# Optimization experiments

Measured on AMD Instinct MI355X. Metric: run time of the kernel, lower is better.

## Reference

```python
import jax, jax.numpy as jnp
import numpy as np

N = 50000
E = 800000
IN_F = 128
HID = 64
CLS = 40


def _seg_softmax(logits, seg, n):
    m = jax.ops.segment_max(logits, seg, num_segments=n)
    e = jnp.exp(logits - m[seg])
    s = jax.ops.segment_sum(e, seg, num_segments=n)
    return e / s[seg]


def _layer(x, src, dst, norm, W, aw, ab, sw, sb, alpha, bias, n):
    h = x @ W.T                                  # [N, HID]
    hs = h[src]                                  # [Etot, HID] gather
    ht = h[dst]
    s = hs * norm[:, None]
    t = ht * norm[:, None]
    s_aggr = jax.ops.segment_sum(hs, src, num_segments=n)
    t_aggr = jax.ops.segment_sum(ht, dst, num_segments=n)
    sim = jax.nn.leaky_relu(
        jnp.concatenate([s, t], axis=-1) @ aw.T + ab, 0.2)[:, 0]
    a = _seg_softmax(sim, src, n)
    nsim = jax.nn.leaky_relu(
        jnp.concatenate([s_aggr[src], t_aggr[dst]], axis=-1) @ sw.T + sb, 0.2)[:, 0]
    struct = _seg_softmax(nsim, src, n)
    w = alpha[0] * a + (1.0 - alpha[0]) * struct  # [Etot]
    msg = w[:, None] * hs                         # message(x_j, norm)
    out = jax.ops.segment_max(msg, dst, num_segments=n)  # aggr='max' at target
    return out + bias


def setup_inputs() -> dict:
    key = jax.random.key(0)
    ks = jax.random.split(key, 16)
    x = jax.random.normal(ks[0], (N, IN_F), dtype=jnp.float32)
    edge_index = jax.random.randint(ks[1], (2, E), 0, N, dtype=jnp.int32)
    norm = jax.random.uniform(ks[2], (E + N,), dtype=jnp.float32)
    def lin(k, o, i):
        return jax.random.normal(k, (o, i), dtype=jnp.float32) / np.sqrt(i)
    return {
        "x": x, "edge_index": edge_index, "norm": norm,
        "lin_w0": lin(ks[3], HID, IN_F), "lin_w1": lin(ks[4], HID, HID),
        "a_w0": lin(ks[5], 1, 2 * HID), "a_b0": jnp.zeros((1,), jnp.float32),
        "a_w1": lin(ks[6], 1, 2 * HID), "a_b1": jnp.zeros((1,), jnp.float32),
        "s_w0": lin(ks[7], 1, 2 * HID), "s_b0": jnp.zeros((1,), jnp.float32),
        "s_w1": lin(ks[8], 1, 2 * HID), "s_b1": jnp.zeros((1,), jnp.float32),
        "alpha0": jnp.array([0.5], jnp.float32), "alpha1": jnp.array([0.5], jnp.float32),
        "bias0": jnp.zeros((HID,), jnp.float32), "bias1": jnp.zeros((HID,), jnp.float32),
        "out_w": lin(ks[9], CLS, HID), "out_b": jnp.zeros((CLS,), jnp.float32),
    }


def reference(x, edge_index, norm, lin_w0, lin_w1, a_w0, a_b0, a_w1, a_b1,
              s_w0, s_b0, s_w1, s_b1, alpha0, alpha1, bias0, bias1, out_w, out_b):
    n = x.shape[0]
    loop = jnp.arange(n, dtype=edge_index.dtype)
    src = jnp.concatenate([edge_index[0], loop])  # add_self_loops
    dst = jnp.concatenate([edge_index[1], loop])
    h = _layer(x, src, dst, norm, lin_w0, a_w0, a_b0, s_w0, s_b0, alpha0, bias0, n)
    h = jax.nn.relu(h)
    h = _layer(h, src, dst, norm, lin_w1, a_w1, a_b1, s_w1, s_b1, alpha1, bias1, n)
    h = jax.nn.relu(h)
    logits = h @ out_w.T + out_b
    return jax.nn.log_softmax(logits, axis=-1)
```

## Files before the change

kernel.cpp:

```cpp
#include <hip/hip_runtime.h>
#include <hip/hip_fp16.h>
#include <cstddef>

#define HID 64
#define CLS 40

__device__ __forceinline__ float lrelu(float x) { return x >= 0.f ? x : 0.2f * x; }

__device__ __forceinline__ float wmax32(float v) {
#pragma unroll
    for (int o = 16; o > 0; o >>= 1) v = fmaxf(v, __shfl_xor(v, o));
    return v;
}
__device__ __forceinline__ float wsum32(float v) {
#pragma unroll
    for (int o = 16; o > 0; o >>= 1) v += __shfl_xor(v, o);
    return v;
}

template <int K, bool APPLY>
__device__ __forceinline__ void gemm_body(const float* __restrict__ X,
                                          const float* __restrict__ W,
                                          const float* __restrict__ aw,
                                          const float* __restrict__ sw,
                                          const int* __restrict__ degS,
                                          const int* __restrict__ degD,
                                          __half* __restrict__ Hh, size_t hN, int R,
                                          float* __restrict__ ds,
                                          float* __restrict__ dssw,
                                          float2* __restrict__ dtp,
                                          float* __restrict__ dtraw,
                                          float* __restrict__ d2raw,
                                          float* __restrict__ d3raw,
                                          int n, int brow, int tid) {
    constexpr int STR = K + 4;
    __shared__ float Wl[HID * STR];
    __shared__ float awl[128];
    __shared__ float swl[128];
    for (int i = tid; i < HID * K; i += 256) {
        int c = i / K, k = i % K;
        Wl[c * STR + k] = W[i];
    }
    if (tid < 128) awl[tid] = aw[tid];
    else swl[tid - 128] = sw[tid - 128];
    __syncthreads();
    int r = brow * 64 + (tid >> 2);
    int seg = tid & 3;
    if (r >= n) return;
    float acc[16];
#pragma unroll
    for (int c = 0; c < 16; c++) acc[c] = 0.f;
    const float* xr = X + (size_t)r * K;
    const float* wb = &Wl[4 * seg * STR];
    for (int k = 0; k < K; k += 4) {
        float4 xv = *reinterpret_cast<const float4*>(xr + k);
#pragma unroll
        for (int c = 0; c < 16; c++) {
            int crel = 16 * (c >> 2) + (c & 3);
            float4 wv = *reinterpret_cast<const float4*>(wb + crel * STR + k);
            acc[c] += xv.x * wv.x + xv.y * wv.y + xv.z * wv.z + xv.w * wv.w;
        }
    }
    float d0 = 0.f, d1 = 0.f, d2 = 0.f, d3 = 0.f;
#pragma unroll
    for (int c = 0; c < 16; c++) {
        int cc = 16 * (c >> 2) + 4 * seg + (c & 3);
        d0 += acc[c] * awl[cc];
        d1 += acc[c] * awl[64 + cc];
        d2 += acc[c] * swl[cc];
        d3 += acc[c] * swl[64 + cc];
    }
    uint2 stv[4];
#pragma unroll
    for (int t = 0; t < 4; t++) {
        union { __half2 h2[2]; uint2 u; } st;
        st.h2[0] = __floats2half2_rn(acc[4 * t], acc[4 * t + 1]);
        st.h2[1] = __floats2half2_rn(acc[4 * t + 2], acc[4 * t + 3]);
        stv[t] = st.u;
    }
    for (int rep = 0; rep < R; rep++) {
        __half* hb = Hh + (size_t)rep * hN + (size_t)r * HID + 4 * seg;
#pragma unroll
        for (int t = 0; t < 4; t++)
            *reinterpret_cast<uint2*>(hb + 16 * t) = stv[t];
    }
    d0 += __shfl_xor(d0, 1); d0 += __shfl_xor(d0, 2);
    d1 += __shfl_xor(d1, 1); d1 += __shfl_xor(d1, 2);
    d2 += __shfl_xor(d2, 1); d2 += __shfl_xor(d2, 2);
    d3 += __shfl_xor(d3, 1); d3 += __shfl_xor(d3, 2);
    if (seg == 0) {
        ds[r] = d0;
        if (APPLY) {
            dssw[r] = (float)(degS[r] + 1) * d2;
            float2 v = make_float2(d1, (float)(degD[r] + 1) * d3);
            for (int rep = 0; rep < 8; rep++) dtp[(size_t)rep * n + r] = v;
        } else {
            dtraw[r] = d1;
            d2raw[r] = d2;
            d3raw[r] = d3;
        }
    }
}

__global__ __launch_bounds__(256) void k_fused0(const float* __restrict__ x,
                                                const float* __restrict__ w0,
                                                const float* __restrict__ aw,
                                                const float* __restrict__ sw,
                                                __half* __restrict__ Hh, size_t hN, int R,
                                                float* __restrict__ ds,
                                                float* __restrict__ dtraw,
                                                float* __restrict__ d2raw,
                                                float* __restrict__ d3raw,
                                                const int* __restrict__ ei,
                                                int* degS, int* degD,
                                                unsigned* __restrict__ ranks,
                                                int n, int E, int gb) {
    if ((int)blockIdx.x < gb) {
        gemm_body<128, false>(x, w0, aw, sw, nullptr, nullptr, Hh, hN, R, ds,
                              nullptr, nullptr, dtraw, d2raw, d3raw,
                              n, blockIdx.x, threadIdx.x);
    } else {
        int t = (blockIdx.x - gb) * 256 + threadIdx.x;
        int stride = (gridDim.x - gb) * 256;
        for (int e = t; e < E; e += stride) {
            int s = ei[e], d = ei[E + e];
            unsigned rs = (unsigned)atomicAdd(&degS[s], 1);
            unsigned rd = (unsigned)atomicAdd(&degD[d], 1);
            ranks[e] = rs | (rd << 16);
        }
    }
}

__global__ __launch_bounds__(256) void k_gemm1(const float* __restrict__ X,
                                               const float* __restrict__ W,
                                               const float* __restrict__ aw,
                                               const float* __restrict__ sw,
                                               const int* __restrict__ degS,
                                               const int* __restrict__ degD,
                                               __half* __restrict__ Hh, size_t hN, int R,
                                               float* __restrict__ ds,
                                               float* __restrict__ dssw,
                                               float2* __restrict__ dtp,
                                               int n) {
    gemm_body<64, true>(X, W, aw, sw, degS, degD, Hh, hN, R, ds, dssw, dtp,
                        nullptr, nullptr, nullptr, n, blockIdx.x, threadIdx.x);
}

__global__ __launch_bounds__(1024) void k_scanA(const int* __restrict__ degS,
                                                const int* __restrict__ degD,
                                                const float* __restrict__ d2raw,
                                                const float* __restrict__ d3raw,
                                                const float* __restrict__ dtraw,
                                                int* __restrict__ offS,
                                                int* __restrict__ offD,
                                                int* __restrict__ bsum,
                                                float* __restrict__ dssw,
                                                float2* __restrict__ dtp,
                                                int n, int nb) {
    __shared__ int buf[2][1024];
    int which = (int)blockIdx.x >= nb;
    const int* deg = which ? degD : degS;
    int* off = which ? offD : offS;
    int b = blockIdx.x - (which ? nb : 0);
    int tid = threadIdx.x;
    int i = b * 1024 + tid;
    int v = (i < n) ? deg[i] + 1 : 0;
    int cur = 0;
    buf[0][tid] = v;
    __syncthreads();
#pragma unroll
    for (int o = 1; o < 1024; o <<= 1) {
        int t = buf[cur][tid];
        if (tid >= o) t += buf[cur][tid - o];
        buf[cur ^ 1][tid] = t;
        cur ^= 1;
        __syncthreads();
    }
    if (i < n) off[i] = buf[cur][tid];
    if (tid == 1023) bsum[which * 64 + b] = buf[cur][1023];
    if (!which && i < n) {
        dssw[i] = (float)(degS[i] + 1) * d2raw[i];
        float2 vv = make_float2(dtraw[i], (float)(degD[i] + 1) * d3raw[i]);
        for (int rep = 0; rep < 8; rep++) dtp[(size_t)rep * n + i] = vv;
    }
}

__global__ __launch_bounds__(1024) void k_scanC(const int* __restrict__ degS,
                                                const int* __restrict__ degD,
                                                int* __restrict__ offS,
                                                int* __restrict__ offD,
                                                const int* __restrict__ bsum,
                                                int n, int total, int nb) {
    __shared__ int basesum;
    int which = (int)blockIdx.x >= nb;
    const int* deg = which ? degD : degS;
    int* off = which ? offD : offS;
    int b = blockIdx.x - (which ? nb : 0);
    if (threadIdx.x < 64) {
        int v = ((int)threadIdx.x < b) ? bsum[which * 64 + threadIdx.x] : 0;
#pragma unroll
        for (int o = 32; o > 0; o >>= 1) v += __shfl_xor(v, o);
        if (threadIdx.x == 0) basesum = v;
    }
    __syncthreads();
    int i = b * 1024 + threadIdx.x;
    if (i < n) off[i] = off[i] - (deg[i] + 1) + basesum;
    if (i == 0) off[n] = total;
}

__global__ __launch_bounds__(256) void k_slots(const int* __restrict__ ei,
                                               const unsigned* __restrict__ ranks,
                                               const int* __restrict__ offS,
                                               const int* __restrict__ offD,
                                               int2* __restrict__ slots,
                                               int Et, int E) {
    int e = blockIdx.x * 256 + threadIdx.x;
    if (e >= Et) return;
    if (e < E) {
        int s = ei[e], d = ei[E + e];
        unsigned ur = ranks[e];
        slots[e] = make_int2(offS[s] + (int)(ur & 0xffffu),
                             offD[d] + (int)(ur >> 16));
    } else {
        int v = e - E;
        slots[e] = make_int2(offS[v + 1] - 1, offD[v + 1] - 1);
    }
}

__global__ __launch_bounds__(256) void k_scatter(const int* __restrict__ ei,
                                                 const float* __restrict__ norm,
                                                 const int2* __restrict__ slots,
                                                 const int* __restrict__ offS,
                                                 const int* __restrict__ offD,
                                                 int2* __restrict__ csrS,
                                                 int2* __restrict__ csrD,
                                                 int Et, int E, int N) {
    int grp = blockIdx.x & 7;
    int lo = (int)(((long long)grp * N) / 8);
    int hi = (int)(((long long)(grp + 1) * N) / 8);
    int sLo = offS[lo], sHi = offS[hi];
    int dLo = offD[lo], dHi = offD[hi];
    int start = (blockIdx.x >> 3) * 256 + threadIdx.x;
    int stride = (gridDim.x >> 3) * 256;
    for (int e = start; e < Et; e += stride) {
        int2 sl = slots[e];
        bool doS = (sl.x >= sLo) & (sl.x < sHi);
        bool doD = (sl.y >= dLo) & (sl.y < dHi);
        if (doS | doD) {
            int nb = __float_as_int(norm[e]);
            if (doS) {
                int d = (e < E) ? ei[E + e] : e - E;
                csrS[sl.x] = make_int2(d, nb);
            }
            if (doD) {
                int s = (e < E) ? ei[e] : e - E;
                csrD[sl.y] = make_int2(s, sl.x);
            }
        }
    }
}

__global__ __launch_bounds__(256) void k_soft(const int* __restrict__ offS,
                                              const int2* __restrict__ csrS,
                                              const float* __restrict__ ds,
                                              const float* __restrict__ dssw,
                                              const float2* __restrict__ dtp,
                                              const float* __restrict__ ab,
                                              const float* __restrict__ sb,
                                              const float* __restrict__ alpha,
                                              float* __restrict__ w, int n) {
    const float2* dtpc = dtp + (size_t)(blockIdx.x & 7) * n;
    int node = blockIdx.x * 8 + (threadIdx.x >> 5);
    int lane = threadIdx.x & 31;
    if (node >= n) return;
    int beg = offS[node];
    int deg = offS[node + 1] - beg;
    float ds_s = ds[node], dssw_s = dssw[node];
    float ab0 = ab[0], sb0 = sb[0], al = alpha[0];

    if (deg <= 32) {
        bool valid = lane < deg;
        float sim = -INFINITY, nsim = -INFINITY;
        int pos = beg + lane;
        if (valid) {
            int2 c = csrS[pos];
            float nr = __int_as_float(c.y);
            float2 p = dtpc[c.x];
            sim = lrelu(nr * (ds_s + p.x) + ab0);
            nsim = lrelu(dssw_s + p.y + sb0);
        }
        float mAv = wmax32(sim), mNv = wmax32(nsim);
        float eA = valid ? expf(sim - mAv) : 0.f;
        float eN = valid ? expf(nsim - mNv) : 0.f;
        float sAv = wsum32(eA), sNv = wsum32(eN);
        if (valid) w[pos] = al * eA / sAv + (1.f - al) * eN / sNv;
    } else {
        float mAv = -INFINITY, mNv = -INFINITY;
        for (int base = 0; base < deg; base += 32) {
            int idx = base + lane;
            if (idx < deg) {
                int2 c = csrS[beg + idx];
                float nr = __int_as_float(c.y);
                float2 p = dtpc[c.x];
                mAv = fmaxf(mAv, lrelu(nr * (ds_s + p.x) + ab0));
                mNv = fmaxf(mNv, lrelu(dssw_s + p.y + sb0));
            }
        }
        mAv = wmax32(mAv);
        mNv = wmax32(mNv);
        float a = 0.f, bb = 0.f;
        for (int base = 0; base < deg; base += 32) {
            int idx = base + lane;
            if (idx < deg) {
                int2 c = csrS[beg + idx];
                float nr = __int_as_float(c.y);
                float2 p = dtpc[c.x];
                a += expf(lrelu(nr * (ds_s + p.x) + ab0) - mAv);
                bb += expf(lrelu(dssw_s + p.y + sb0) - mNv);
            }
        }
        float sAv = wsum32(a);
        float sNv = wsum32(bb);
        for (int base = 0; base < deg; base += 32) {
            int idx = base + lane;
            if (idx < deg) {
                int2 c = csrS[beg + idx];
                float nr = __int_as_float(c.y);
                float2 p = dtpc[c.x];
                float eA = expf(lrelu(nr * (ds_s + p.x) + ab0) - mAv);
                float eN = expf(lrelu(dssw_s + p.y + sb0) - mNv);
                w[beg + idx] = al * eA / sAv + (1.f - al) * eN / sNv;
            }
        }
    }
}

__global__ __launch_bounds__(256) void k_aggr(const int* __restrict__ offD,
                                              const int2* __restrict__ csrD,
                                              const float* __restrict__ w,
                                              const __half* __restrict__ HhR,
                                              size_t hN, int R,
                                              const float* __restrict__ bias,
                                              float* __restrict__ out, int n) {
    const __half* Hh = HhR + (size_t)(blockIdx.x & (R - 1)) * hN;
    int wid = threadIdx.x >> 6;
    int lane = threadIdx.x & 63;
    int half = lane >> 5;
    int l32 = lane & 31;
    int node = (blockIdx.x * 4 + wid) * 2 + half;
    bool nvalid = node < n;
    int beg = 0, deg = 0;
    if (nvalid) { beg = offD[node]; deg = offD[node + 1] - beg; }
    int degOther = __shfl(deg, lane ^ 32);
    int maxdeg = max(deg, degOther);
    float ml0 = -INFINITY, ml1 = -INFINITY, ml2 = -INFINITY, ml3 = -INFINITY;
    float mh0 = -INFINITY, mh1 = -INFINITY, mh2 = -INFINITY, mh3 = -INFINITY;
    for (int base = 0; base < maxdeg; base += 32) {
        int idx = base + l32;
        int s = 0;
        float wv = 0.f;
        if (idx < deg) {
            int2 c = csrD[beg + idx];
            s = c.x;
            wv = w[c.y];
        }
        int cnt = min(32, maxdeg - base);
        int cnt4 = cnt & ~3;
        int bl = half << 5;
        for (int j = 0; j < cnt4; j += 4) {
            int s0 = __shfl(s, bl + j),     s1 = __shfl(s, bl + j + 1),
                s2 = __shfl(s, bl + j + 2), s3 = __shfl(s, bl + j + 3);
            float w0 = __shfl(wv, bl + j),     w1 = __shfl(wv, bl + j + 1),
                  w2 = __shfl(wv, bl + j + 2), w3 = __shfl(wv, bl + j + 3);
            float hl0 = __half2float(Hh[(size_t)s0 * HID + l32]);
            float hh0 = __half2float(Hh[(size_t)s0 * HID + 32 + l32]);
            float hl1 = __half2float(Hh[(size_t)s1 * HID + l32]);
            float hh1 = __half2float(Hh[(size_t)s1 * HID + 32 + l32]);
            float hl2 = __half2float(Hh[(size_t)s2 * HID + l32]);
            float hh2 = __half2float(Hh[(size_t)s2 * HID + 32 + l32]);
            float hl3 = __half2float(Hh[(size_t)s3 * HID + l32]);
            float hh3 = __half2float(Hh[(size_t)s3 * HID + 32 + l32]);
            if (base + j < deg)     { ml0 = fmaxf(ml0, w0 * hl0); mh0 = fmaxf(mh0, w0 * hh0); }
            if (base + j + 1 < deg) { ml1 = fmaxf(ml1, w1 * hl1); mh1 = fmaxf(mh1, w1 * hh1); }
            if (base + j + 2 < deg) { ml2 = fmaxf(ml2, w2 * hl2); mh2 = fmaxf(mh2, w2 * hh2); }
            if (base + j + 3 < deg) { ml3 = fmaxf(ml3, w3 * hl3); mh3 = fmaxf(mh3, w3 * hh3); }
        }
        for (int j = cnt4; j < cnt; j++) {
            int sj = __shfl(s, bl + j);
            float wj = __shfl(wv, bl + j);
            float hl = __half2float(Hh[(size_t)sj * HID + l32]);
            float hh = __half2float(Hh[(size_t)sj * HID + 32 + l32]);
            if (base + j < deg) { ml0 = fmaxf(ml0, wj * hl); mh0 = fmaxf(mh0, wj * hh); }
        }
    }
    if (nvalid) {
        float mlo = fmaxf(fmaxf(ml0, ml1), fmaxf(ml2, ml3));
        float mhi = fmaxf(fmaxf(mh0, mh1), fmaxf(mh2, mh3));
        out[(size_t)node * HID + l32] = fmaxf(mlo + bias[l32], 0.f);
        out[(size_t)node * HID + 32 + l32] = fmaxf(mhi + bias[32 + l32], 0.f);
    }
}

__global__ __launch_bounds__(256) void k_logits(const float* __restrict__ H,
                                                const float* __restrict__ OW,
                                                const float* __restrict__ OB,
                                                float* __restrict__ out, int n) {
    __shared__ float Wl[CLS * HID];
    __shared__ float Bl[CLS];
    int tid = threadIdx.x;
    for (int i = tid; i < CLS * HID; i += 256) Wl[i] = OW[i];
    if (tid < CLS) Bl[tid] = OB[tid];
    __syncthreads();
    int node = blockIdx.x * 32 + (tid >> 3);
    int g = tid & 7;
    if (node >= n) return;
    const float* h = H + (size_t)node * HID;
    float hreg[HID];
#pragma unroll
    for (int k = 0; k < HID; k += 4) {
        float4 hv = *reinterpret_cast<const float4*>(h + k);
        hreg[k] = hv.x; hreg[k + 1] = hv.y; hreg[k + 2] = hv.z; hreg[k + 3] = hv.w;
    }
    float lg[5];
#pragma unroll
    for (int j = 0; j < 5; j++) {
        int c = g * 5 + j;
        float a = 0.f;
        const float* wr = &Wl[c * HID];
#pragma unroll
        for (int k = 0; k < HID; k++) a += hreg[k] * wr[k];
        lg[j] = a + Bl[c];
    }
    float m = lg[0];
#pragma unroll
    for (int j = 1; j < 5; j++) m = fmaxf(m, lg[j]);
    m = fmaxf(m, __shfl_xor(m, 1));
    m = fmaxf(m, __shfl_xor(m, 2));
    m = fmaxf(m, __shfl_xor(m, 4));
    float s = 0.f;
#pragma unroll
    for (int j = 0; j < 5; j++) s += expf(lg[j] - m);
    s += __shfl_xor(s, 1);
    s += __shfl_xor(s, 2);
    s += __shfl_xor(s, 4);
    float lse = m + logf(s);
    float* o = out + (size_t)node * CLS + g * 5;
#pragma unroll
    for (int j = 0; j < 5; j++) o[j] = lg[j] - lse;
}

extern "C" void kernel_launch(void* const* d_in, const int* in_sizes, int n_in,
                              void* d_out, int out_size, void* d_ws, size_t ws_size,
                              hipStream_t stream) {
    const float* x   = (const float*)d_in[0];
    const int*   ei  = (const int*)d_in[1];
    const float* nrm = (const float*)d_in[2];
    const float* w0  = (const float*)d_in[3];
    const float* w1  = (const float*)d_in[4];
    const float* aw0 = (const float*)d_in[5];
    const float* ab0 = (const float*)d_in[6];
    const float* aw1 = (const float*)d_in[7];
    const float* ab1 = (const float*)d_in[8];
    const float* sw0 = (const float*)d_in[9];
    const float* sb0 = (const float*)d_in[10];
    const float* sw1 = (const float*)d_in[11];
    const float* sb1 = (const float*)d_in[12];
    const float* al0 = (const float*)d_in[13];
    const float* al1 = (const float*)d_in[14];
    const float* b0  = (const float*)d_in[15];
    const float* b1  = (const float*)d_in[16];
    const float* ow  = (const float*)d_in[17];
    const float* ob  = (const float*)d_in[18];
    float* out = (float*)d_out;

    int N = in_sizes[0] / 128;
    int E = in_sizes[1] / 2;
    int Et = E + N;

    char* base = (char*)d_ws;
    size_t off = 0;
    auto alloc = [&](size_t bytes) {
        void* p = base + off;
        off += (bytes + 255) & ~(size_t)255;
        return p;
    };
    int* degS = (int*)alloc(N * 4);
    int* degD = (int*)alloc(N * 4);
    int* offS = (int*)alloc((N + 1) * 4);
    int* offD = (int*)alloc((N + 1) * 4);
    int* bsum = (int*)alloc(128 * 4);
    unsigned* ranks = (unsigned*)alloc((size_t)E * 4);
    int2* slots = (int2*)alloc((size_t)Et * 8);
    int2* csrS = (int2*)alloc((size_t)Et * 8);
    int2* csrD = (int2*)alloc((size_t)Et * 8);
    float* wgt   = (float*)alloc((size_t)Et * 4);
    float* ds    = (float*)alloc(N * 4);
    float* dssw  = (float*)alloc(N * 4);
    float* dtraw = (float*)alloc(N * 4);
    float* d2raw = (float*)alloc(N * 4);
    float* d3raw = (float*)alloc(N * 4);
    float2* dtp  = (float2*)alloc((size_t)N * 8 * 8);
    float* lay   = (float*)alloc((size_t)N * HID * 4);

    size_t hbytes = (size_t)N * HID * 2;
    size_t rem = (off < ws_size) ? ws_size - off : hbytes;
    int R = 1;
    while (R < 8 && (size_t)(R * 2) * hbytes <= rem) R <<= 1;
    __half* HhR = (__half*)alloc(hbytes * R);
    size_t hN = (size_t)N * HID;

    int nbScan = (N + 1023) / 1024;
    int nbW2 = (N + 7) / 8;
    int nbS = (N + 7) / 8;
    int gb = (N + 63) / 64;
    int cnb = (E + 1023) / 1024;

    hipMemsetAsync(degS, 0, (size_t)N * 4, stream);
    hipMemsetAsync(degD, 0, (size_t)N * 4, stream);
    k_fused0<<<gb + cnb, 256, 0, stream>>>(x, w0, aw0, sw0, HhR, hN, R, ds,
                                           dtraw, d2raw, d3raw,
                                           ei, degS, degD, ranks, N, E, gb);
    k_scanA<<<2 * nbScan, 1024, 0, stream>>>(degS, degD, d2raw, d3raw, dtraw,
                                             offS, offD, bsum, dssw, dtp,
                                             N, nbScan);
    k_scanC<<<2 * nbScan, 1024, 0, stream>>>(degS, degD, offS, offD, bsum,
                                             N, Et, nbScan);
    k_slots<<<(Et + 255) / 256, 256, 0, stream>>>(ei, ranks, offS, offD,
                                                  slots, Et, E);
    k_scatter<<<2048, 256, 0, stream>>>(ei, nrm, slots, offS, offD,
                                        csrS, csrD, Et, E, N);

    k_soft<<<nbS, 256, 0, stream>>>(offS, csrS, ds, dssw, dtp,
                                    ab0, sb0, al0, wgt, N);
    k_aggr<<<nbW2, 256, 0, stream>>>(offD, csrD, wgt, HhR, hN, R, b0, lay, N);

    k_gemm1<<<gb, 256, 0, stream>>>(lay, w1, aw1, sw1, degS, degD,
                                    HhR, hN, R, ds, dssw, dtp, N);
    k_soft<<<nbS, 256, 0, stream>>>(offS, csrS, ds, dssw, dtp,
                                    ab1, sb1, al1, wgt, N);
    k_aggr<<<nbW2, 256, 0, stream>>>(offD, csrD, wgt, HhR, hN, R, b1, lay, N);

    k_logits<<<(N + 31) / 32, 256, 0, stream>>>(lay, ow, ob, out, N);
}
```

Measured before the change: 294.0 us.

## Fuse logits into final aggregation, store edge weights and layer output in fp16

Edge weights are now stored as fp16 and replicated R times alongside the replicated H copies, so each aggr block reads from its own replica. The layer-1 output is stored as fp16 and read by gemm1 through a half-precision load path. The separate logits/log-softmax kernel is folded into the second aggregation kernel, which computes the output projection from shared memory. This cuts memory traffic and one launch, at the cost of precision loss in weights and activations, more replicated-write work in k_soft, and an extra block-wide sync in the final aggregation.

```diff
diff --git a/kernel.cpp b/kernel.cpp
--- a/kernel.cpp
+++ b/kernel.cpp
@@ -18,8 +18,8 @@
     return v;
 }
 
-template <int K, bool APPLY>
-__device__ __forceinline__ void gemm_body(const float* __restrict__ X,
+template <int K, bool APPLY, typename XT>
+__device__ __forceinline__ void gemm_body(const XT* __restrict__ X,
                                           const float* __restrict__ W,
                                           const float* __restrict__ aw,
                                           const float* __restrict__ sw,
@@ -50,10 +50,18 @@
     float acc[16];
 #pragma unroll
     for (int c = 0; c < 16; c++) acc[c] = 0.f;
-    const float* xr = X + (size_t)r * K;
+    const XT* xr = X + (size_t)r * K;
     const float* wb = &Wl[4 * seg * STR];
     for (int k = 0; k < K; k += 4) {
-        float4 xv = *reinterpret_cast<const float4*>(xr + k);
+        float4 xv;
+        if constexpr (sizeof(XT) == 4) {
+            xv = *reinterpret_cast<const float4*>(xr + k);
+        } else {
+            __half2 a = *reinterpret_cast<const __half2*>(xr + k);
+            __half2 b = *reinterpret_cast<const __half2*>(xr + k + 2);
+            xv = make_float4(__low2float(a), __high2float(a),
+                             __low2float(b), __high2float(b));
+        }
 #pragma unroll
         for (int c = 0; c < 16; c++) {
             int crel = 16 * (c >> 2) + (c & 3);
@@ -116,9 +124,9 @@
                                                 unsigned* __restrict__ ranks,
                                                 int n, int E, int gb) {
     if ((int)blockIdx.x < gb) {
-        gemm_body<128, false>(x, w0, aw, sw, nullptr, nullptr, Hh, hN, R, ds,
-                              nullptr, nullptr, dtraw, d2raw, d3raw,
-                              n, blockIdx.x, threadIdx.x);
+        gemm_body<128, false, float>(x, w0, aw, sw, nullptr, nullptr, Hh, hN, R, ds,
+                                     nullptr, nullptr, dtraw, d2raw, d3raw,
+                                     n, blockIdx.x, threadIdx.x);
     } else {
         int t = (blockIdx.x - gb) * 256 + threadIdx.x;
         int stride = (gridDim.x - gb) * 256;
@@ -131,7 +139,7 @@
     }
 }
 
-__global__ __launch_bounds__(256) void k_gemm1(const float* __restrict__ X,
+__global__ __launch_bounds__(256) void k_gemm1(const __half* __restrict__ X,
                                                const float* __restrict__ W,
                                                const float* __restrict__ aw,
                                                const float* __restrict__ sw,
@@ -142,8 +150,8 @@
                                                float* __restrict__ dssw,
                                                float2* __restrict__ dtp,
                                                int n) {
-    gemm_body<64, true>(X, W, aw, sw, degS, degD, Hh, hN, R, ds, dssw, dtp,
-                        nullptr, nullptr, nullptr, n, blockIdx.x, threadIdx.x);
+    gemm_body<64, true, __half>(X, W, aw, sw, degS, degD, Hh, hN, R, ds, dssw, dtp,
+                                nullptr, nullptr, nullptr, n, blockIdx.x, threadIdx.x);
 }
 
 __global__ __launch_bounds__(1024) void k_scanA(const int* __restrict__ degS,
@@ -268,7 +276,8 @@
                                               const float* __restrict__ ab,
                                               const float* __restrict__ sb,
                                               const float* __restrict__ alpha,
-                                              float* __restrict__ w, int n) {
+                                              __half* __restrict__ wgtR, int wN, int R,
+                                              int n) {
     const float2* dtpc = dtp + (size_t)(blockIdx.x & 7) * n;
     int node = blockIdx.x * 8 + (threadIdx.x >> 5);
     int lane = threadIdx.x & 31;
@@ -293,7 +302,10 @@
         float eA = valid ? expf(sim - mAv) : 0.f;
         float eN = valid ? expf(nsim - mNv) : 0.f;
         float sAv = wsum32(eA), sNv = wsum32(eN);
-        if (valid) w[pos] = al * eA / sAv + (1.f - al) * eN / sNv;
+        if (valid) {
+            __half hv = __float2half(al * eA / sAv + (1.f - al) * eN / sNv);
+            for (int rep = 0; rep < R; rep++) wgtR[(size_t)rep * wN + pos] = hv;
+        }
     } else {
         float mAv = -INFINITY, mNv = -INFINITY;
         for (int base = 0; base < deg; base += 32) {
@@ -329,24 +341,42 @@
                 float2 p = dtpc[c.x];
                 float eA = expf(lrelu(nr * (ds_s + p.x) + ab0) - mAv);
                 float eN = expf(lrelu(dssw_s + p.y + sb0) - mNv);
-                w[beg + idx] = al * eA / sAv + (1.f - al) * eN / sNv;
+                __half hv = __float2half(al * eA / sAv + (1.f - al) * eN / sNv);
+                for (int rep = 0; rep < R; rep++)
+                    wgtR[(size_t)rep * wN + beg + idx] = hv;
             }
         }
     }
 }
 
+template <bool FINAL>
 __global__ __launch_bounds__(256) void k_aggr(const int* __restrict__ offD,
                                               const int2* __restrict__ csrD,
-                                              const float* __restrict__ w,
-                                              const __half* __restrict__ HhR,
-                                              size_t hN, int R,
+                                              const __half* __restrict__ wgtR, int wN,
+                                              const __half* __restrict__ HhR, size_t hN,
+                                              int R,
                                               const float* __restrict__ bias,
-                                              float* __restrict__ out, int n) {
-    const __half* Hh = HhR + (size_t)(blockIdx.x & (R - 1)) * hN;
+                                              const float* __restrict__ OW,
+                                              const float* __restrict__ OB,
+                                              __half* __restrict__ outH,
+                                              float* __restrict__ outF, int n) {
+    __shared__ float WlT[FINAL ? HID * CLS : 1];
+    __shared__ float Bl[FINAL ? CLS : 1];
+    __shared__ float hbuf[FINAL ? 8 : 1][FINAL ? HID : 1];
+    if (FINAL) {
+        for (int i = threadIdx.x; i < CLS * HID; i += 256)
+            WlT[(i & (HID - 1)) * CLS + (i >> 6)] = OW[i];
+        if (threadIdx.x < CLS) Bl[threadIdx.x] = OB[threadIdx.x];
+        __syncthreads();
+    }
+    int cpy = blockIdx.x & (R - 1);
+    const __half* Hh = HhR + (size_t)cpy * hN;
+    const __half* wg = wgtR + (size_t)cpy * wN;
     int wid = threadIdx.x >> 6;
     int lane = threadIdx.x & 63;
     int half = lane >> 5;
     int l32 = lane & 31;
+    int halfId = threadIdx.x >> 5;
     int node = (blockIdx.x * 4 + wid) * 2 + half;
     bool nvalid = node < n;
     int beg = 0, deg = 0;
@@ -362,7 +392,7 @@
         if (idx < deg) {
             int2 c = csrD[beg + idx];
             s = c.x;
-            wv = w[c.y];
+            wv = __half2float(wg[c.y]);
         }
         int cnt = min(32, maxdeg - base);
         int cnt4 = cnt & ~3;
@@ -393,60 +423,34 @@
             if (base + j < deg) { ml0 = fmaxf(ml0, wj * hl); mh0 = fmaxf(mh0, wj * hh); }
         }
     }
-    if (nvalid) {
-        float mlo = fmaxf(fmaxf(ml0, ml1), fmaxf(ml2, ml3));
-        float mhi = fmaxf(fmaxf(mh0, mh1), fmaxf(mh2, mh3));
-        out[(size_t)node * HID + l32] = fmaxf(mlo + bias[l32], 0.f);
-        out[(size_t)node * HID + 32 + l32] = fmaxf(mhi + bias[32 + l32], 0.f);
-    }
-}
-
-__global__ __launch_bounds__(256) void k_logits(const float* __restrict__ H,
-                                                const float* __restrict__ OW,
-                                                const float* __restrict__ OB,
-                                                float* __restrict__ out, int n) {
-    __shared__ float Wl[CLS * HID];
-    __shared__ float Bl[CLS];
-    int tid = threadIdx.x;
-    for (int i = tid; i < CLS * HID; i += 256) Wl[i] = OW[i];
-    if (tid < CLS) Bl[tid] = OB[tid];
-    __syncthreads();
-    int node = blockIdx.x * 32 + (tid >> 3);
-    int g = tid & 7;
-    if (node >= n) return;
-    const float* h = H + (size_t)node * HID;
-    float hreg[HID];
-#pragma unroll
-    for (int k = 0; k < HID; k += 4) {
-        float4 hv = *reinterpret_cast<const float4*>(h + k);
-        hreg[k] = hv.x; hreg[k + 1] = hv.y; hreg[k + 2] = hv.z; hreg[k + 3] = hv.w;
-    }
-    float lg[5];
-#pragma unroll
-    for (int j = 0; j < 5; j++) {
-        int c = g * 5 + j;
-        float a = 0.f;
-        const float* wr = &Wl[c * HID];
-#pragma unroll
-        for (int k = 0; k < HID; k++) a += hreg[k] * wr[k];
-        lg[j] = a + Bl[c];
-    }
-    float m = lg[0];
-#pragma unroll
-    for (int j = 1; j < 5; j++) m = fmaxf(m, lg[j]);
-    m = fmaxf(m, __shfl_xor(m, 1));
-    m = fmaxf(m, __shfl_xor(m, 2));
-    m = fmaxf(m, __shfl_xor(m, 4));
-    float s = 0.f;
-#pragma unroll
-    for (int j = 0; j < 5; j++) s += expf(lg[j] - m);
-    s += __shfl_xor(s, 1);
-    s += __shfl_xor(s, 2);
-    s += __shfl_xor(s, 4);
-    float lse = m + logf(s);
-    float* o = out + (size_t)node * CLS + g * 5;
-#pragma unroll
-    for (int j = 0; j < 5; j++) o[j] = lg[j] - lse;
+    float mlo = fmaxf(fmaxf(ml0, ml1), fmaxf(ml2, ml3));
+    float mhi = fmaxf(fmaxf(mh0, mh1), fmaxf(mh2, mh3));
+    float vlo = fmaxf(mlo + bias[l32], 0.f);
+    float vhi = fmaxf(mhi + bias[32 + l32], 0.f);
+    if (!FINAL) {
+        if (nvalid) {
+            outH[(size_t)node * HID + l32] = __float2half(vlo);
+            outH[(size_t)node * HID + 32 + l32] = __float2half(vhi);
+        }
+    } else {
+        hbuf[halfId][l32] = nvalid ? vlo : 0.f;
+        hbuf[halfId][32 + l32] = nvalid ? vhi : 0.f;
+        __syncthreads();
+        float lg1 = Bl[l32];
+        float lg2 = (l32 < 8) ? Bl[32 + l32] : -INFINITY;
+        for (int k = 0; k < HID; k++) {
+            float hv = hbuf[halfId][k];
+            lg1 += hv * WlT[k * CLS + l32];
+            if (l32 < 8) lg2 += hv * WlT[k * CLS + 32 + l32];
+        }
+        float m = wmax32(fmaxf(lg1, lg2));
+        float ssum = wsum32(expf(lg1 - m) + ((l32 < 8) ? expf(lg2 - m) : 0.f));
+        float lse = m + logf(ssum);
+        if (nvalid) {
+            outF[(size_t)node * CLS + l32] = lg1 - lse;
+            if (l32 < 8) outF[(size_t)node * CLS + 32 + l32] = lg2 - lse;
+        }
+    }
 }
 
 extern "C" void kernel_launch(void* const* d_in, const int* in_sizes, int n_in,
@@ -493,20 +497,21 @@
     int2* slots = (int2*)alloc((size_t)Et * 8);
     int2* csrS = (int2*)alloc((size_t)Et * 8);
     int2* csrD = (int2*)alloc((size_t)Et * 8);
-    float* wgt   = (float*)alloc((size_t)Et * 4);
     float* ds    = (float*)alloc(N * 4);
     float* dssw  = (float*)alloc(N * 4);
     float* dtraw = (float*)alloc(N * 4);
     float* d2raw = (float*)alloc(N * 4);
     float* d3raw = (float*)alloc(N * 4);
     float2* dtp  = (float2*)alloc((size_t)N * 8 * 8);
-    float* lay   = (float*)alloc((size_t)N * HID * 4);
+    __half* layh = (__half*)alloc((size_t)N * HID * 2);
 
     size_t hbytes = (size_t)N * HID * 2;
-    size_t rem = (off < ws_size) ? ws_size - off : hbytes;
+    size_t wbytes = (size_t)Et * 2;
+    size_t rem = (ws_size > off) ? ws_size - off : (hbytes + wbytes);
     int R = 1;
-    while (R < 8 && (size_t)(R * 2) * hbytes <= rem) R <<= 1;
-    __half* HhR = (__half*)alloc(hbytes * R);
+    while (R < 8 && (size_t)(2 * R) * (hbytes + wbytes) <= rem) R <<= 1;
+    __half* HhR  = (__half*)alloc(hbytes * R);
+    __half* wgtR = (__half*)alloc(wbytes * R);
     size_t hN = (size_t)N * HID;
 
     int nbScan = (N + 1023) / 1024;
@@ -531,14 +536,14 @@
                                         csrS, csrD, Et, E, N);
 
     k_soft<<<nbS, 256, 0, stream>>>(offS, csrS, ds, dssw, dtp,
-                                    ab0, sb0, al0, wgt, N);
-    k_aggr<<<nbW2, 256, 0, stream>>>(offD, csrD, wgt, HhR, hN, R, b0, lay, N);
-
-    k_gemm1<<<gb, 256, 0, stream>>>(lay, w1, aw1, sw1, degS, degD,
+                                    ab0, sb0, al0, wgtR, Et, R, N);
+    k_aggr<false><<<nbW2, 256, 0, stream>>>(offD, csrD, wgtR, Et, HhR, hN, R,
+                                            b0, nullptr, nullptr, layh, nullptr, N);
+
+    k_gemm1<<<gb, 256, 0, stream>>>(layh, w1, aw1, sw1, degS, degD,
                                     HhR, hN, R, ds, dssw, dtp, N);
     k_soft<<<nbS, 256, 0, stream>>>(offS, csrS, ds, dssw, dtp,
-                                    ab1, sb1, al1, wgt, N);
-    k_aggr<<<nbW2, 256, 0, stream>>>(offD, csrD, wgt, HhR, hN, R, b1, lay, N);
-
-    k_logits<<<(N + 31) / 32, 256, 0, stream>>>(lay, ow, ob, out, N);
-}
+                                    ab1, sb1, al1, wgtR, Et, R, N);
+    k_aggr<true><<<nbW2, 256, 0, stream>>>(offD, csrD, wgtR, Et, HhR, hN, R,
+                                           b1, ow, ob, nullptr, out, N);
+}
```

Result: faster. 262.8 us (-10.6%).
